# Performance work log

Hardware: AMD Instinct MI355X
Metric: run time of the kernel (lower is better)

Reference implementation:

```python
import jax, jax.numpy as jnp
import numpy as np

EPS = 1e-5  # rms_norm_eps

def rmsnorm(x, w, eps=EPS):
    xf = x.astype(jnp.float32)
    n = xf * jax.lax.rsqrt(jnp.mean(xf * xf, axis=-1, keepdims=True) + eps)
    return n.astype(x.dtype) * w

def setup_inputs() -> dict:
    key = jax.random.key(0)
    ks = jax.random.split(key, 8)
    B, S, E = 2, 2048, 2048
    H, M, D = 16, 2048, 128  # heads, memory slots, head_dim; H*D == E
    return {
        "query": jax.random.normal(ks[0], (B, S, E), jnp.float32),
        "storedpatterns": jax.random.normal(ks[1], (H, M, D), jnp.float32) * 0.02,
        "wq": jax.random.normal(ks[2], (H * D, E), jnp.float32) * (1.0 / np.sqrt(E)),
        "wk": jax.random.normal(ks[3], (D, D), jnp.float32) * (1.0 / np.sqrt(D)),
        "wv": jax.random.normal(ks[4], (D, D), jnp.float32) * (1.0 / np.sqrt(D)),
        "beta": jnp.ones((1, H, 1, 1), jnp.float32),
        "norm_q_w": jnp.ones((E,), jnp.float32),
        "norm_r_w": jnp.ones((H * D,), jnp.float32),
    }

def reference(query, storedpatterns, wq, wk, wv, beta, norm_q_w, norm_r_w):
    B, S, E = query.shape
    H, M, D = storedpatterns.shape
    # RMSNorm query, project to multi-head queries [B,H,S,D]
    qn = rmsnorm(query, norm_q_w)
    q = jnp.einsum('bse,fe->bsf', qn, wq).reshape(B, S, H, D).transpose(0, 2, 1, 3)
    # per-head K/V projections of stored memory patterns [H,M,D]
    k = jnp.einsum('hmd,ed->hme', storedpatterns, wk)
    v = jnp.einsum('hmd,ed->hme', storedpatterns, wv)
    # beta-scaled attention over memory slots
    scores = jnp.einsum('bhsd,hmd->bhsm', q, k) * beta / jnp.sqrt(jnp.float32(D))
    attn = jax.nn.softmax(scores, axis=-1)
    retrieved = jnp.einsum('bhsm,hmd->bhsd', attn, v)  # [B,H,S,D]
    retrieved = retrieved.transpose(0, 2, 1, 3).reshape(B, S, H * D)
    retrieved = rmsnorm(retrieved, norm_r_w)
    # combine_method='add' (pattern_dim == emb_dim, no dim projection)
    return query + retrieved
```

## Files before the change

### kernel.cpp

```cpp
#include <hip/hip_runtime.h>
#include <hip/hip_bf16.h>
#include <stdint.h>

typedef __attribute__((ext_vector_type(8))) short bf16x8;
typedef __attribute__((ext_vector_type(4))) float f32x4;
typedef __attribute__((ext_vector_type(8))) unsigned short u16x8;
typedef __attribute__((ext_vector_type(4))) unsigned short u16x4;
typedef __attribute__((ext_vector_type(2))) unsigned long long ull2;
typedef __attribute__((ext_vector_type(8))) int i32x8;

#define B_ 2
#define S_ 2048
#define E_ 2048
#define H_ 16
#define M_ 2048
#define D_ 128

#define MFMA16(a, b, c) __builtin_amdgcn_mfma_f32_16x16x32_bf16(a, b, c, 0, 0, 0)
#define MFMA8(a, b, c) __builtin_amdgcn_mfma_f32_16x16x32_fp8_fp8(a, b, c, 0, 0, 0)
#define MFMAS(a, b, c) __builtin_amdgcn_mfma_scale_f32_16x16x128_f8f6f4( \
    a, b, c, 0, 0, 0, 127, 0, 127)

union U32x8 { ull2 u2[2]; long long q[4]; i32x8 v; };

__device__ inline unsigned short f2bf(float f) {
  union { float f; unsigned u; } v; v.f = f;
  unsigned r = v.u + 0x7FFFu + ((v.u >> 16) & 1u);
  return (unsigned short)(r >> 16);
}
__device__ inline float bf2f(unsigned short h) {
  union { unsigned u; float f; } v; v.u = ((unsigned)h) << 16;
  return v.f;
}

__device__ inline unsigned char f2e8(float f) {
  return (unsigned char)(__builtin_amdgcn_cvt_pk_fp8_f32(f, f, 0, false) & 0xFF);
}
__device__ inline uint32_t pk4e8(float a, float b, float c, float d) {
  uint32_t w = 0;
  w = (uint32_t)__builtin_amdgcn_cvt_pk_fp8_f32(a, b, (int)w, false);
  w = (uint32_t)__builtin_amdgcn_cvt_pk_fp8_f32(c, d, (int)w, true);
  return w;
}

__device__ inline float exp2a(float x) {
  float r;
  asm("v_exp_f32 %0, %1" : "=v"(r) : "v"(x));
  return r;
}

__device__ inline void gload_lds16(const void* g, void* l) {
  __builtin_amdgcn_global_load_lds(
      (__attribute__((address_space(1))) void*)g,
      (__attribute__((address_space(3))) void*)l, 16, 0, 0);
}

__device__ inline bf16x8 pack8(float4 f0, float4 f1) {
  bf16x8 o;
  o[0] = (short)f2bf(f0.x); o[1] = (short)f2bf(f0.y);
  o[2] = (short)f2bf(f0.z); o[3] = (short)f2bf(f0.w);
  o[4] = (short)f2bf(f1.x); o[5] = (short)f2bf(f1.y);
  o[6] = (short)f2bf(f1.z); o[7] = (short)f2bf(f1.w);
  return o;
}

__device__ inline float block_sum(float v) {
  __shared__ float red[4];
  #pragma unroll
  for (int o = 32; o > 0; o >>= 1) v += __shfl_xor(v, o);
  int tid = threadIdx.x;
  if ((tid & 63) == 0) red[tid >> 6] = v;
  __syncthreads();
  return red[0] + red[1] + red[2] + red[3];
}

__device__ inline int pi_pos(int c) {
  return (c & ~127) | (((c >> 3) & 3) * 32) | (((c >> 5) & 3) * 8) | (c & 7);
}

#define PREP_PROJ 512
#define PREP_CONV 2048
#define PREP_NORM 4096
__global__ __launch_bounds__(256, 2) void prep_kernel(
    const float* __restrict__ query, const float* __restrict__ sp,
    const float* __restrict__ wq, const float* __restrict__ wk,
    const float* __restrict__ wv, const float* __restrict__ nqw,
    unsigned char* __restrict__ wqb, unsigned char* __restrict__ qn,
    unsigned char* __restrict__ kout, unsigned char* __restrict__ vtout)
{
  const int bid = blockIdx.x;
  const int tid = threadIdx.x;

  if (bid < PREP_PROJ) {
    const int idx = bid;
    const int m0 = (idx & 31) * 64;
    const int h = idx >> 5;
    const int wave = tid >> 6, lane = tid & 63;
    const int r = lane & 15, g = lane >> 4;
    const int wm = (wave >> 1) * 32, wn = (wave & 1) * 64;
    const float* spb = sp + ((size_t)h * M_ + m0) * D_;
    f32x4 acck[2][4] = {};
    f32x4 accv[2][4] = {};
    #pragma unroll
    for (int kc = 0; kc < 4; ++kc) {
      bf16x8 a[2], bk[4], bv[4];
      #pragma unroll
      for (int m = 0; m < 2; ++m) {
        const float* p = spb + (size_t)(wm + m * 16 + r) * D_ + kc * 32 + g * 8;
        a[m] = pack8(*(const float4*)p, *(const float4*)(p + 4));
      }
      #pragma unroll
      for (int n = 0; n < 4; ++n) {
        const float* pk = wk + (size_t)(wn + n * 16 + r) * D_ + kc * 32 + g * 8;
        bk[n] = pack8(*(const float4*)pk, *(const float4*)(pk + 4));
        const float* pv = wv + (size_t)(wn + n * 16 + r) * D_ + kc * 32 + g * 8;
        bv[n] = pack8(*(const float4*)pv, *(const float4*)(pv + 4));
      }
      #pragma unroll
      for (int m = 0; m < 2; ++m)
        #pragma unroll
        for (int n = 0; n < 4; ++n) {
          acck[m][n] = MFMA16(a[m], bk[n], acck[m][n]);
          accv[m][n] = MFMA16(a[m], bv[n], accv[m][n]);
        }
    }
    #pragma unroll
    for (int m = 0; m < 2; ++m)
      #pragma unroll
      for (int n = 0; n < 4; ++n)
        #pragma unroll
        for (int i = 0; i < 4; ++i) {
          int d = wn + n * 16 + r;
          kout[((size_t)h * M_ + m0 + wm + m * 16 + g * 4 + i) * D_ + pi_pos(d)]
              = f2e8(acck[m][n][i] * 32.0f);
          int mc = m0 + wm + m * 16 + g * 4 + i;
          int mp = (mc & ~127) | (pi_pos(mc & 127));
          vtout[((size_t)h * D_ + wn + n * 16 + r) * M_ + mp]
              = f2e8(accv[m][n][i] * 32.0f);
        }
  } else if (bid < PREP_PROJ + PREP_CONV) {
    int i = (bid - PREP_PROJ) * 256 + tid;
    const float* p = wq + (size_t)i * 8;
    float4 a = *(const float4*)p, b = *(const float4*)(p + 4);
    uint2 pk;
    pk.x = pk4e8(a.x, a.y, a.z, a.w);
    pk.y = pk4e8(b.x, b.y, b.z, b.w);
    size_t flat = (size_t)i * 8;
    int c = (int)(flat & (E_ - 1));
    *(uint2*)(wqb + (flat - c) + pi_pos(c)) = pk;
  } else {
    const int row = bid - (PREP_PROJ + PREP_CONV);
    const float* xr = query + (size_t)row * E_;
    float4 v0 = ((const float4*)xr)[tid * 2];
    float4 v1 = ((const float4*)xr)[tid * 2 + 1];
    float ss = v0.x*v0.x + v0.y*v0.y + v0.z*v0.z + v0.w*v0.w
             + v1.x*v1.x + v1.y*v1.y + v1.z*v1.z + v1.w*v1.w;
    float tot = block_sum(ss);
    float sc = rsqrtf(tot * (1.0f / E_) + 1e-5f);
    float vals[8] = {v0.x, v0.y, v0.z, v0.w, v1.x, v1.y, v1.z, v1.w};
    const float* wr = nqw + tid * 8;
    float f[8];
    #pragma unroll
    for (int j = 0; j < 8; ++j) f[j] = vals[j] * sc * wr[j];
    uint2 pk;
    pk.x = pk4e8(f[0], f[1], f[2], f[3]);
    pk.y = pk4e8(f[4], f[5], f[6], f[7]);
    *(uint2*)(qn + (size_t)row * E_ + pi_pos(tid * 8)) = pk;
  }
}

__global__ __launch_bounds__(256) void gemm_qproj(
    const unsigned char* __restrict__ A, const unsigned char* __restrict__ B,
    unsigned char* __restrict__ C, int M, int N, int K)
{
  __shared__ __align__(16) unsigned char As[128 * 128];
  __shared__ __align__(16) unsigned char Bs[128 * 128];
  const int nwg = gridDim.x;
  const int cpx = nwg >> 3;
  const int swz = (blockIdx.x & 7) * cpx + (blockIdx.x >> 3);
  const int mt = M >> 7;
  const int bm = (swz % mt) * 128;
  const int bn = (swz / mt) * 128;
  const int tid = threadIdx.x;
  const int wave = tid >> 6, lane = tid & 63;
  const int r = lane & 15, g = lane >> 4;
  const int wm = (wave >> 1) * 64, wn = (wave & 1) * 64;
  const int fx = (r & 7) << 4;

  f32x4 acc[4][4] = {};

  for (int k0 = 0; k0 < K; k0 += 128) {
    #pragma unroll
    for (int c = 0; c < 4; ++c) {
      int chunk = wave * 4 + c;
      int off = chunk * 1024 + lane * 16;
      int row = off >> 7;
      int cb = (off & 127) ^ ((row & 7) << 4);
      gload_lds16(A + (size_t)(bm + row) * K + k0 + cb, (char*)As + chunk * 1024);
      gload_lds16(B + (size_t)(bn + row) * K + k0 + cb, (char*)Bs + chunk * 1024);
    }
    __syncthreads();
    {
      U32x8 af[4], bf[4];
      #pragma unroll
      for (int m = 0; m < 4; ++m) {
        const char* pr = (const char*)As + (wm + m * 16 + r) * 128;
        af[m].u2[0] = *(const ull2*)(pr + ((g * 32) ^ fx));
        af[m].u2[1] = *(const ull2*)(pr + ((g * 32 + 16) ^ fx));
      }
      #pragma unroll
      for (int n = 0; n < 4; ++n) {
        const char* pr = (const char*)Bs + (wn + n * 16 + r) * 128;
        bf[n].u2[0] = *(const ull2*)(pr + ((g * 32) ^ fx));
        bf[n].u2[1] = *(const ull2*)(pr + ((g * 32 + 16) ^ fx));
      }
      #pragma unroll
      for (int m = 0; m < 4; ++m)
        #pragma unroll
        for (int n = 0; n < 4; ++n)
          acc[m][n] = MFMAS(af[m].v, bf[n].v, acc[m][n]);
    }
    __syncthreads();
  }
  #pragma unroll
  for (int m = 0; m < 4; ++m)
    #pragma unroll
    for (int n = 0; n < 4; ++n)
      #pragma unroll
      for (int i = 0; i < 4; ++i) {
        int row = bm + wm + m * 16 + g * 4 + i;
        int col = bn + wn + n * 16 + r;
        C[(size_t)row * N + col] = f2e8(acc[m][n][i]);
      }
}

__global__ __launch_bounds__(256, 2) void attn_kernel(
    const unsigned char* __restrict__ q,
    const unsigned char* __restrict__ kb,
    const unsigned char* __restrict__ vtb,
    const float* __restrict__ beta,
    unsigned short* __restrict__ ret)
{
  __shared__ __align__(16) unsigned char Ks[2][128 * 128];
  __shared__ __align__(16) unsigned char Vs[2][128 * 128];
  __shared__ __align__(16) unsigned char Ps[4][32 * 128];
  const int s0 = blockIdx.x * 128;
  const int h = blockIdx.y;
  const int b = blockIdx.z;
  const int tid = threadIdx.x, wave = tid >> 6, lane = tid & 63;
  const int r = lane & 15, g = lane >> 4;
  const int fx = (r & 7) << 4;
  const float escale = beta[h] * (0.08838834764831845f * 1.4426950408889634f / 32.0f);

  U32x8 qv0, qv1;
  {
    const unsigned char* qr0 =
        q + ((size_t)(b * S_) + s0 + wave * 16 + r) * E_ + h * D_;
    const unsigned char* qr1 = qr0 + (size_t)64 * E_;
    #pragma unroll
    for (int kc = 0; kc < 4; ++kc) {
      qv0.q[kc] = *(const long long*)(qr0 + kc * 32 + g * 8);
      qv1.q[kc] = *(const long long*)(qr1 + kc * 32 + g * 8);
    }
  }

  const unsigned char* Kh = kb + (size_t)h * M_ * D_;
  const unsigned char* Vh = vtb + (size_t)h * D_ * M_;
  unsigned char* Pw = Ps[wave];
  U32x8 ones8;
  #pragma unroll
  for (int i = 0; i < 4; ++i) ones8.q[i] = 0x3838383838383838LL;

  f32x4 o0[8] = {}, o1[8] = {};
  f32x4 ol0 = {}, ol1 = {};

  auto stage = [&](int buf, int m0) {
    #pragma unroll
    for (int c = 0; c < 4; ++c) {
      int chunk = wave * 4 + c;
      int off = chunk * 1024 + lane * 16;
      int row = off >> 7;
      int cb = (off & 127) ^ ((row & 7) << 4);
      gload_lds16(Kh + (size_t)(m0 + row) * 128 + cb, (char*)Ks[buf] + chunk * 1024);
      gload_lds16(Vh + (size_t)row * M_ + m0 + cb, (char*)Vs[buf] + chunk * 1024);
    }
  };

  stage(0, 0);
  __syncthreads();

  int cur = 0;
  for (int t = 0; t < M_ / 128; ++t) {
    if (t + 1 < M_ / 128) stage(cur ^ 1, (t + 1) * 128);

    const unsigned char* Kc = Ks[cur];
    const unsigned char* Vc = Vs[cur];

    f32x4 sA[8] = {}, sB[8] = {};
    __builtin_amdgcn_s_setprio(1);
    #pragma unroll
    for (int nf = 0; nf < 8; ++nf) {
      const unsigned char* kr = Kc + (nf * 16 + r) * 128;
      U32x8 kf;
      kf.u2[0] = *(const ull2*)(kr + ((g * 32) ^ fx));
      kf.u2[1] = *(const ull2*)(kr + ((g * 32 + 16) ^ fx));
      sA[nf] = MFMAS(kf.v, qv0.v, sA[nf]);
      sB[nf] = MFMAS(kf.v, qv1.v, sB[nf]);
    }
    __builtin_amdgcn_s_setprio(0);

    #pragma unroll
    for (int nf = 0; nf < 8; ++nf) {
      int pbase = ((nf & 1) * 2 + (g >> 1)) * 32 + (nf >> 1) * 8 + (g & 1) * 4;
      {
        float p0 = exp2a(sA[nf][0] * escale), p1 = exp2a(sA[nf][1] * escale),
              p2 = exp2a(sA[nf][2] * escale), p3 = exp2a(sA[nf][3] * escale);
        *(uint32_t*)(Pw + r * 128 + (pbase ^ fx)) = pk4e8(p0, p1, p2, p3);
      }
      {
        float p0 = exp2a(sB[nf][0] * escale), p1 = exp2a(sB[nf][1] * escale),
              p2 = exp2a(sB[nf][2] * escale), p3 = exp2a(sB[nf][3] * escale);
        *(uint32_t*)(Pw + (16 + r) * 128 + (pbase ^ fx)) = pk4e8(p0, p1, p2, p3);
      }
    }

    U32x8 pv0, pv1;
    pv0.u2[0] = *(const ull2*)(Pw + r * 128 + ((g * 32) ^ fx));
    pv0.u2[1] = *(const ull2*)(Pw + r * 128 + ((g * 32 + 16) ^ fx));
    pv1.u2[0] = *(const ull2*)(Pw + (16 + r) * 128 + ((g * 32) ^ fx));
    pv1.u2[1] = *(const ull2*)(Pw + (16 + r) * 128 + ((g * 32 + 16) ^ fx));
    __builtin_amdgcn_s_setprio(1);
    ol0 = MFMAS(pv0.v, ones8.v, ol0);
    ol1 = MFMAS(pv1.v, ones8.v, ol1);
    #pragma unroll
    for (int nf2 = 0; nf2 < 8; ++nf2) {
      const unsigned char* vr = Vc + (nf2 * 16 + r) * 128;
      U32x8 vf;
      vf.u2[0] = *(const ull2*)(vr + ((g * 32) ^ fx));
      vf.u2[1] = *(const ull2*)(vr + ((g * 32 + 16) ^ fx));
      o0[nf2] = MFMAS(pv0.v, vf.v, o0[nf2]);
      o1[nf2] = MFMAS(pv1.v, vf.v, o1[nf2]);
    }
    __builtin_amdgcn_s_setprio(0);
    __syncthreads();
    cur ^= 1;
  }

  {
    float inv[4];
    #pragma unroll
    for (int i = 0; i < 4; ++i) inv[i] = 0.03125f / ol0[i];
    unsigned short* rr = ret + ((size_t)(b * S_) + s0 + wave * 16) * E_ + h * D_;
    #pragma unroll
    for (int nf2 = 0; nf2 < 8; ++nf2)
      #pragma unroll
      for (int i = 0; i < 4; ++i)
        rr[(size_t)(g * 4 + i) * E_ + nf2 * 16 + r] = f2bf(o0[nf2][i] * inv[i]);
  }
  {
    float inv[4];
    #pragma unroll
    for (int i = 0; i < 4; ++i) inv[i] = 0.03125f / ol1[i];
    unsigned short* rr = ret + ((size_t)(b * S_) + s0 + 64 + wave * 16) * E_ + h * D_;
    #pragma unroll
    for (int nf2 = 0; nf2 < 8; ++nf2)
      #pragma unroll
      for (int i = 0; i < 4; ++i)
        rr[(size_t)(g * 4 + i) * E_ + nf2 * 16 + r] = f2bf(o1[nf2][i] * inv[i]);
  }
}

__global__ __launch_bounds__(256) void final_kernel(
    const unsigned short* __restrict__ ret, const float* __restrict__ w,
    const float* __restrict__ query, float* __restrict__ out)
{
  const int row = blockIdx.x;
  const int tid = threadIdx.x;
  u16x8 hv = *(const u16x8*)(ret + (size_t)row * E_ + tid * 8);
  float x[8];
  float ss = 0.f;
  #pragma unroll
  for (int j = 0; j < 8; ++j) { x[j] = bf2f(hv[j]); ss += x[j] * x[j]; }
  float tot = block_sum(ss);
  float sc = rsqrtf(tot * (1.0f / E_) + 1e-5f);
  const float* qr = query + (size_t)row * E_ + tid * 8;
  const float* wr = w + tid * 8;
  float o[8];
  #pragma unroll
  for (int j = 0; j < 8; ++j) o[j] = qr[j] + x[j] * sc * wr[j];
  float4* op = (float4*)(out + (size_t)row * E_ + tid * 8);
  op[0] = make_float4(o[0], o[1], o[2], o[3]);
  op[1] = make_float4(o[4], o[5], o[6], o[7]);
}

extern "C" void kernel_launch(void* const* d_in, const int* in_sizes, int n_in,
                              void* d_out, int out_size, void* d_ws, size_t ws_size,
                              hipStream_t stream) {
  const float* query = (const float*)d_in[0];
  const float* sp    = (const float*)d_in[1];
  const float* wq    = (const float*)d_in[2];
  const float* wk    = (const float*)d_in[3];
  const float* wv    = (const float*)d_in[4];
  const float* beta  = (const float*)d_in[5];
  const float* nqw   = (const float*)d_in[6];
  const float* nrw   = (const float*)d_in[7];
  float* out = (float*)d_out;

  char* ws = (char*)d_ws;
  unsigned char*  wqb = (unsigned char*)(ws + 0);
  unsigned char*  qn  = (unsigned char*)(ws + ((size_t)8 << 20));
  unsigned char*  qb  = (unsigned char*)(ws + ((size_t)24 << 20));
  unsigned char*  kb  = (unsigned char*)(ws + ((size_t)32 << 20));
  unsigned char*  vtb = (unsigned char*)(ws + ((size_t)36 << 20));
  unsigned short* ret = (unsigned short*)(ws + ((size_t)40 << 20));

  prep_kernel<<<PREP_PROJ + PREP_CONV + PREP_NORM, 256, 0, stream>>>(
      query, sp, wq, wk, wv, nqw, wqb, qn, kb, vtb);
  gemm_qproj<<<(B_ * S_ / 128) * (E_ / 128), 256, 0, stream>>>(
      qn, wqb, qb, B_ * S_, E_, E_);
  attn_kernel<<<dim3(S_ / 128, H_, B_), 256, 0, stream>>>(qb, kb, vtb, beta, ret);
  final_kernel<<<B_ * S_, 256, 0, stream>>>(ret, nrw, query, out);
}
```

Measured before the change: 120.1 us.

## Move K/V projection blocks from prep kernel into the Q-projection GEMM launch

The per-head K/V projection of stored patterns now runs as extra workgroups in the Q-projection GEMM launch instead of in the prep kernel. Since the K/V work does not depend on the normalized queries, it can fill idle compute units alongside the GEMM tiles (512 GEMM blocks on a 256-CU device leaves a tail). This also makes the prep kernel lighter, so it no longer needs the MFMA path or the 2-blocks-per-CU launch bound. The cost is a combined kernel whose register and LDS use are sized for the larger GEMM branch, which can lower occupancy for the K/V blocks.

```diff
diff --git a/kernel.cpp b/kernel.cpp
--- a/kernel.cpp
+++ b/kernel.cpp
@@ -78,68 +78,18 @@
   return (c & ~127) | (((c >> 3) & 3) * 32) | (((c >> 5) & 3) * 8) | (c & 7);
 }
 
-#define PREP_PROJ 512
 #define PREP_CONV 2048
 #define PREP_NORM 4096
-__global__ __launch_bounds__(256, 2) void prep_kernel(
-    const float* __restrict__ query, const float* __restrict__ sp,
-    const float* __restrict__ wq, const float* __restrict__ wk,
-    const float* __restrict__ wv, const float* __restrict__ nqw,
-    unsigned char* __restrict__ wqb, unsigned char* __restrict__ qn,
-    unsigned char* __restrict__ kout, unsigned char* __restrict__ vtout)
+__global__ __launch_bounds__(256) void prep_kernel(
+    const float* __restrict__ query, const float* __restrict__ wq,
+    const float* __restrict__ nqw,
+    unsigned char* __restrict__ wqb, unsigned char* __restrict__ qn)
 {
   const int bid = blockIdx.x;
   const int tid = threadIdx.x;
 
-  if (bid < PREP_PROJ) {
-    const int idx = bid;
-    const int m0 = (idx & 31) * 64;
-    const int h = idx >> 5;
-    const int wave = tid >> 6, lane = tid & 63;
-    const int r = lane & 15, g = lane >> 4;
-    const int wm = (wave >> 1) * 32, wn = (wave & 1) * 64;
-    const float* spb = sp + ((size_t)h * M_ + m0) * D_;
-    f32x4 acck[2][4] = {};
-    f32x4 accv[2][4] = {};
-    #pragma unroll
-    for (int kc = 0; kc < 4; ++kc) {
-      bf16x8 a[2], bk[4], bv[4];
-      #pragma unroll
-      for (int m = 0; m < 2; ++m) {
-        const float* p = spb + (size_t)(wm + m * 16 + r) * D_ + kc * 32 + g * 8;
-        a[m] = pack8(*(const float4*)p, *(const float4*)(p + 4));
-      }
-      #pragma unroll
-      for (int n = 0; n < 4; ++n) {
-        const float* pk = wk + (size_t)(wn + n * 16 + r) * D_ + kc * 32 + g * 8;
-        bk[n] = pack8(*(const float4*)pk, *(const float4*)(pk + 4));
-        const float* pv = wv + (size_t)(wn + n * 16 + r) * D_ + kc * 32 + g * 8;
-        bv[n] = pack8(*(const float4*)pv, *(const float4*)(pv + 4));
-      }
-      #pragma unroll
-      for (int m = 0; m < 2; ++m)
-        #pragma unroll
-        for (int n = 0; n < 4; ++n) {
-          acck[m][n] = MFMA16(a[m], bk[n], acck[m][n]);
-          accv[m][n] = MFMA16(a[m], bv[n], accv[m][n]);
-        }
-    }
-    #pragma unroll
-    for (int m = 0; m < 2; ++m)
-      #pragma unroll
-      for (int n = 0; n < 4; ++n)
-        #pragma unroll
-        for (int i = 0; i < 4; ++i) {
-          int d = wn + n * 16 + r;
-          kout[((size_t)h * M_ + m0 + wm + m * 16 + g * 4 + i) * D_ + pi_pos(d)]
-              = f2e8(acck[m][n][i] * 32.0f);
-          int mc = m0 + wm + m * 16 + g * 4 + i;
-          int mp = (mc & ~127) | (pi_pos(mc & 127));
-          vtout[((size_t)h * D_ + wn + n * 16 + r) * M_ + mp]
-              = f2e8(accv[m][n][i] * 32.0f);
-        }
-  } else if (bid < PREP_PROJ + PREP_CONV) {
-    int i = (bid - PREP_PROJ) * 256 + tid;
+  if (bid < PREP_CONV) {
+    int i = bid * 256 + tid;
     const float* p = wq + (size_t)i * 8;
     float4 a = *(const float4*)p, b = *(const float4*)(p + 4);
     uint2 pk;
@@ -149,7 +99,7 @@
     int c = (int)(flat & (E_ - 1));
     *(uint2*)(wqb + (flat - c) + pi_pos(c)) = pk;
   } else {
-    const int row = bid - (PREP_PROJ + PREP_CONV);
+    const int row = bid - PREP_CONV;
     const float* xr = query + (size_t)row * E_;
     float4 v0 = ((const float4*)xr)[tid * 2];
     float4 v1 = ((const float4*)xr)[tid * 2 + 1];
@@ -169,69 +119,121 @@
   }
 }
 
-__global__ __launch_bounds__(256) void gemm_qproj(
-    const unsigned char* __restrict__ A, const unsigned char* __restrict__ B,
-    unsigned char* __restrict__ C, int M, int N, int K)
+#define GEMM_WG 512
+__global__ __launch_bounds__(256) void gemm_proj_kernel(
+    const unsigned char* __restrict__ A, const unsigned char* __restrict__ Bm,
+    unsigned char* __restrict__ C,
+    const float* __restrict__ sp, const float* __restrict__ wk,
+    const float* __restrict__ wv,
+    unsigned char* __restrict__ kout, unsigned char* __restrict__ vtout)
 {
   __shared__ __align__(16) unsigned char As[128 * 128];
   __shared__ __align__(16) unsigned char Bs[128 * 128];
-  const int nwg = gridDim.x;
-  const int cpx = nwg >> 3;
-  const int swz = (blockIdx.x & 7) * cpx + (blockIdx.x >> 3);
-  const int mt = M >> 7;
-  const int bm = (swz % mt) * 128;
-  const int bn = (swz / mt) * 128;
   const int tid = threadIdx.x;
   const int wave = tid >> 6, lane = tid & 63;
   const int r = lane & 15, g = lane >> 4;
-  const int wm = (wave >> 1) * 64, wn = (wave & 1) * 64;
   const int fx = (r & 7) << 4;
 
-  f32x4 acc[4][4] = {};
-
-  for (int k0 = 0; k0 < K; k0 += 128) {
-    #pragma unroll
-    for (int c = 0; c < 4; ++c) {
-      int chunk = wave * 4 + c;
-      int off = chunk * 1024 + lane * 16;
-      int row = off >> 7;
-      int cb = (off & 127) ^ ((row & 7) << 4);
-      gload_lds16(A + (size_t)(bm + row) * K + k0 + cb, (char*)As + chunk * 1024);
-      gload_lds16(B + (size_t)(bn + row) * K + k0 + cb, (char*)Bs + chunk * 1024);
-    }
-    __syncthreads();
-    {
-      U32x8 af[4], bf[4];
-      #pragma unroll
-      for (int m = 0; m < 4; ++m) {
-        const char* pr = (const char*)As + (wm + m * 16 + r) * 128;
-        af[m].u2[0] = *(const ull2*)(pr + ((g * 32) ^ fx));
-        af[m].u2[1] = *(const ull2*)(pr + ((g * 32 + 16) ^ fx));
+  if (blockIdx.x < GEMM_WG) {
+    const int M = B_ * S_, N = E_, K = E_;
+    const int cpx = GEMM_WG >> 3;
+    const int swz = (blockIdx.x & 7) * cpx + (blockIdx.x >> 3);
+    const int mt = M >> 7;
+    const int bm = (swz % mt) * 128;
+    const int bn = (swz / mt) * 128;
+    const int wm = (wave >> 1) * 64, wn = (wave & 1) * 64;
+
+    f32x4 acc[4][4] = {};
+
+    for (int k0 = 0; k0 < K; k0 += 128) {
+      #pragma unroll
+      for (int c = 0; c < 4; ++c) {
+        int chunk = wave * 4 + c;
+        int off = chunk * 1024 + lane * 16;
+        int row = off >> 7;
+        int cb = (off & 127) ^ ((row & 7) << 4);
+        gload_lds16(A + (size_t)(bm + row) * K + k0 + cb, (char*)As + chunk * 1024);
+        gload_lds16(Bm + (size_t)(bn + row) * K + k0 + cb, (char*)Bs + chunk * 1024);
+      }
+      __syncthreads();
+      {
+        U32x8 af[4], bf[4];
+        #pragma unroll
+        for (int m = 0; m < 4; ++m) {
+          const char* pr = (const char*)As + (wm + m * 16 + r) * 128;
+          af[m].u2[0] = *(const ull2*)(pr + ((g * 32) ^ fx));
+          af[m].u2[1] = *(const ull2*)(pr + ((g * 32 + 16) ^ fx));
+        }
+        #pragma unroll
+        for (int n = 0; n < 4; ++n) {
+          const char* pr = (const char*)Bs + (wn + n * 16 + r) * 128;
+          bf[n].u2[0] = *(const ull2*)(pr + ((g * 32) ^ fx));
+          bf[n].u2[1] = *(const ull2*)(pr + ((g * 32 + 16) ^ fx));
+        }
+        #pragma unroll
+        for (int m = 0; m < 4; ++m)
+          #pragma unroll
+          for (int n = 0; n < 4; ++n)
+            acc[m][n] = MFMAS(af[m].v, bf[n].v, acc[m][n]);
+      }
+      __syncthreads();
+    }
+    #pragma unroll
+    for (int m = 0; m < 4; ++m)
+      #pragma unroll
+      for (int n = 0; n < 4; ++n)
+        #pragma unroll
+        for (int i = 0; i < 4; ++i) {
+          int row = bm + wm + m * 16 + g * 4 + i;
+          int col = bn + wn + n * 16 + r;
+          C[(size_t)row * N + col] = f2e8(acc[m][n][i]);
+        }
+  } else {
+    const int idx = blockIdx.x - GEMM_WG;
+    const int m0 = (idx & 31) * 64;
+    const int h = idx >> 5;
+    const int wm = (wave >> 1) * 32, wn = (wave & 1) * 64;
+    const float* spb = sp + ((size_t)h * M_ + m0) * D_;
+    f32x4 acck[2][4] = {};
+    f32x4 accv[2][4] = {};
+    #pragma unroll
+    for (int kc = 0; kc < 4; ++kc) {
+      bf16x8 a[2], bk[4], bv[4];
+      #pragma unroll
+      for (int m = 0; m < 2; ++m) {
+        const float* p = spb + (size_t)(wm + m * 16 + r) * D_ + kc * 32 + g * 8;
+        a[m] = pack8(*(const float4*)p, *(const float4*)(p + 4));
       }
       #pragma unroll
       for (int n = 0; n < 4; ++n) {
-        const char* pr = (const char*)Bs + (wn + n * 16 + r) * 128;
-        bf[n].u2[0] = *(const ull2*)(pr + ((g * 32) ^ fx));
-        bf[n].u2[1] = *(const ull2*)(pr + ((g * 32 + 16) ^ fx));
-      }
-      #pragma unroll
-      for (int m = 0; m < 4; ++m)
-        #pragma unroll
-        for (int n = 0; n < 4; ++n)
-          acc[m][n] = MFMAS(af[m].v, bf[n].v, acc[m][n]);
-    }
-    __syncthreads();
-  }
-  #pragma unroll
-  for (int m = 0; m < 4; ++m)
-    #pragma unroll
-    for (int n = 0; n < 4; ++n)
-      #pragma unroll
-      for (int i = 0; i < 4; ++i) {
-        int row = bm + wm + m * 16 + g * 4 + i;
-        int col = bn + wn + n * 16 + r;
-        C[(size_t)row * N + col] = f2e8(acc[m][n][i]);
-      }
+        const float* pk = wk + (size_t)(wn + n * 16 + r) * D_ + kc * 32 + g * 8;
+        bk[n] = pack8(*(const float4*)pk, *(const float4*)(pk + 4));
+        const float* pv = wv + (size_t)(wn + n * 16 + r) * D_ + kc * 32 + g * 8;
+        bv[n] = pack8(*(const float4*)pv, *(const float4*)(pv + 4));
+      }
+      #pragma unroll
+      for (int m = 0; m < 2; ++m)
+        #pragma unroll
+        for (int n = 0; n < 4; ++n) {
+          acck[m][n] = MFMA16(a[m], bk[n], acck[m][n]);
+          accv[m][n] = MFMA16(a[m], bv[n], accv[m][n]);
+        }
+    }
+    #pragma unroll
+    for (int m = 0; m < 2; ++m)
+      #pragma unroll
+      for (int n = 0; n < 4; ++n)
+        #pragma unroll
+        for (int i = 0; i < 4; ++i) {
+          int d = wn + n * 16 + r;
+          kout[((size_t)h * M_ + m0 + wm + m * 16 + g * 4 + i) * D_ + pi_pos(d)]
+              = f2e8(acck[m][n][i] * 32.0f);
+          int mc = m0 + wm + m * 16 + g * 4 + i;
+          int mp = (mc & ~127) | (pi_pos(mc & 127));
+          vtout[((size_t)h * D_ + wn + n * 16 + r) * M_ + mp]
+              = f2e8(accv[m][n][i] * 32.0f);
+        }
+  }
 }
 
 __global__ __launch_bounds__(256, 2) void attn_kernel(
@@ -414,10 +416,9 @@
   unsigned char*  vtb = (unsigned char*)(ws + ((size_t)36 << 20));
   unsigned short* ret = (unsigned short*)(ws + ((size_t)40 << 20));
 
-  prep_kernel<<<PREP_PROJ + PREP_CONV + PREP_NORM, 256, 0, stream>>>(
-      query, sp, wq, wk, wv, nqw, wqb, qn, kb, vtb);
-  gemm_qproj<<<(B_ * S_ / 128) * (E_ / 128), 256, 0, stream>>>(
-      qn, wqb, qb, B_ * S_, E_, E_);
+  prep_kernel<<<PREP_CONV + PREP_NORM, 256, 0, stream>>>(query, wq, nqw, wqb, qn);
+  gemm_proj_kernel<<<GEMM_WG + 512, 256, 0, stream>>>(
+      qn, wqb, qb, sp, wk, wv, kb, vtb);
   attn_kernel<<<dim3(S_ / 128, H_, B_), 256, 0, stream>>>(qb, kb, vtb, beta, ret);
   final_kernel<<<B_ * S_, 256, 0, stream>>>(ret, nrw, query, out);
 }
```

After: 116.5 us (median of 2 runs). 1.03x faster.
